# Optimization experiments

Hardware: AMD Instinct MI355X
Metric: run time of the kernel (lower is better)

Reference implementation:

```python
import jax, jax.numpy as jnp
import numpy as np

N_LOCAL = 16                      # top-k cone hits per (anchor, query)
COS_TH = float(np.cos(np.pi / 12))  # cone half-angle threshold: th = pi / cone_angle_th, cone_angle_th=12


def setup_inputs() -> dict:
    key = jax.random.key(0)
    k1, k2, k3 = jax.random.split(key, 3)
    pcd = jax.random.normal(k1, (2, 2048, 3), dtype=jnp.float32)  # point cloud
    qry = jax.random.normal(k2, (2, 512, 3), dtype=jnp.float32)   # query points
    anc = jax.random.normal(k3, (2, 48, 3), dtype=jnp.float32)    # anchors
    return {"pcd": pcd, "qry": qry, "anc": anc}


def reference(pcd, qry, anc):
    """Cone-cast top-k neighbor search + relative-feature computation of ARONetModel
    (cast_cone + cal_relatives with norm_coord=False), fully vectorized over anchors.

    Returns a single packed array [b, n_qry, n_anc, 1 + n_local, 4]:
      slot 0 along axis 3 is feat_anc2qry, slots 1..k are feat_qry2hit.
    """
    # ---- cast_cone (vectorized over the anchor loop of the original) ----
    # anchor->point distances/directions do NOT depend on the query, so compute once.
    vec_ap = pcd[:, None, :, :] - anc[:, :, None, :]            # [b,a,p,3]
    dist_ap = jnp.linalg.norm(vec_ap, axis=-1)                  # [b,a,p]
    dir_ap = vec_ap / dist_ap[..., None]                        # [b,a,p,3]

    vec_aq = qry[:, None, :, :] - anc[:, :, None, :]            # [b,a,q,3]
    dir_aq = vec_aq / jnp.linalg.norm(vec_aq, axis=-1, keepdims=True)

    # cosine between anchor->query ray and anchor->point directions
    cos = jnp.einsum('baqd,bapd->baqp', dir_aq, dir_ap)         # [b,a,q,p]
    # points outside the cone get distance +inf (torch: mod[flt_angle] = inf)
    masked = jnp.where(cos <= COS_TH, jnp.inf, dist_ap[:, :, None, :])  # [b,a,q,p]

    neg_vals, idx = jax.lax.top_k(-masked, N_LOCAL)             # smallest-k distances
    vals = -neg_vals                                            # [b,a,q,k]

    # gather the hit point coordinates
    hit_raw = jnp.take_along_axis(pcd[:, None, None, :, :], idx[..., None], axis=3)  # [b,a,q,k,3]
    # padded (no valid point in cone) -> replace with the query point itself
    pad = jnp.isinf(vals)[..., None]                            # [b,a,q,k,1]
    hit = jnp.where(pad, qry[:, None, :, None, :], hit_raw)     # [b,a,q,k,3]
    hit = jnp.transpose(hit, (0, 2, 1, 3, 4))                   # [b,q,a,k,3]

    # ---- cal_relatives (norm_coord = False) ----
    vec_qa = qry[:, :, None, :] - anc[:, None, :, :]            # [b,q,a,3]
    mod_qa = jnp.linalg.norm(vec_qa, axis=-1, keepdims=True)    # [b,q,a,1]
    feat_anc2qry = jnp.concatenate([vec_qa, mod_qa], axis=-1)   # [b,q,a,4]

    vec_qh = hit - qry[:, :, None, None, :]                     # [b,q,a,k,3]
    sq = jnp.sum(vec_qh * vec_qh, axis=-1, keepdims=True)       # [b,q,a,k,1]
    zero = sq == 0.0                                            # padded hits -> exact zero
    mod_qh = jnp.where(zero, 0.0, jnp.sqrt(jnp.where(zero, 1.0, sq)))
    feat_qry2hit = jnp.concatenate([vec_qh, mod_qh], axis=-1)   # [b,q,a,k,4]

    # pack both outputs into one array: [b,q,a,1+k,4]
    return jnp.concatenate([feat_anc2qry[:, :, :, None, :], feat_qry2hit], axis=3)
```

## Files before the change

kernel.cpp:

```cpp
#include <hip/hip_runtime.h>

#define P_N 2048
#define Q_N 512
#define A_N 48
#define WPTS 512
#define CHUNK 256
#define CAP 24
#define LSTR 25

__device__ __forceinline__ float dot3_rn(float ax, float ay, float az,
                                         float bx, float by, float bz) {
    return __fadd_rn(__fadd_rn(__fmul_rn(ax, bx), __fmul_rn(ay, by)),
                     __fmul_rn(az, bz));
}

__device__ __forceinline__ float dot3_fma(float ax, float ay, float az,
                                          float bx, float by, float bz) {
    return __fmaf_rn(az, bz, __fmaf_rn(ay, by, __fmul_rn(ax, bx)));
}

__device__ __forceinline__ void insert16(float d, int idx, float (&td)[16], int (&ti)[16]) {
    if (d >= td[15]) return;
    #pragma unroll
    for (int j = 15; j >= 1; --j) {
        float oldd = td[j]; int oldi = ti[j];
        bool up   = (d < td[j - 1]);
        bool here = (d < oldd);
        td[j] = up ? td[j - 1] : (here ? d : oldd);
        ti[j] = up ? ti[j - 1] : (here ? idx : oldi);
    }
    if (d < td[0]) { ti[0] = idx; td[0] = d; }
}

__global__ __launch_bounds__(256, 4) void aronet_kernel(
        const float* __restrict__ pcd, const float* __restrict__ qry,
        const float* __restrict__ anc, float* __restrict__ out) {
    __shared__ float4 spt[P_N];
    __shared__ unsigned char cand[256 * LSTR];

    uint2* mbuf = (uint2*)spt;

    const int tid  = threadIdx.x;
    const int lane = tid & 63;
    const int w    = tid >> 6;

    const int bid = blockIdx.x;
    const int qc  = bid & 7;
    const int ba  = bid >> 3;
    const int a   = ba % A_N;
    const int b   = ba / A_N;

    const float ax = anc[(b * A_N + a) * 3 + 0];
    const float ay = anc[(b * A_N + a) * 3 + 1];
    const float az = anc[(b * A_N + a) * 3 + 2];

    const float* pbase = pcd + (size_t)b * P_N * 3;
    const int pq0 = w * WPTS;
    for (int i = lane; i < WPTS; i += 64) {
        const int p = pq0 + i;
        float vx = __fsub_rn(pbase[p * 3 + 0], ax);
        float vy = __fsub_rn(pbase[p * 3 + 1], ay);
        float vz = __fsub_rn(pbase[p * 3 + 2], az);
        float d2 = dot3_rn(vx, vy, vz, vx, vy, vz);
        float dist = __fsqrt_rn(d2);
        float r = __fdiv_rn(1.0f, dist);
        spt[p] = make_float4(dist, __fmul_rn(vx, r), __fmul_rn(vy, r), __fmul_rn(vz, r));
    }

    const int q = (qc << 6) + lane;
    const float qx = qry[((size_t)b * Q_N + q) * 3 + 0];
    const float qy = qry[((size_t)b * Q_N + q) * 3 + 1];
    const float qz = qry[((size_t)b * Q_N + q) * 3 + 2];
    const float vqx = __fsub_rn(qx, ax);
    const float vqy = __fsub_rn(qy, ay);
    const float vqz = __fsub_rn(qz, az);
    const float qd2 = dot3_rn(vqx, vqy, vqz, vqx, vqy, vqz);
    const float qdist = __fsqrt_rn(qd2);
    const float qr = __fdiv_rn(1.0f, qdist);
    const float dqx = __fmul_rn(vqx, qr);
    const float dqy = __fmul_rn(vqy, qr);
    const float dqz = __fmul_rn(vqz, qr);

    const float COS_TH = 0.9659258262890683f;

    float td[16]; int ti[16];
    #pragma unroll
    for (int j = 0; j < 16; ++j) { td[j] = __builtin_inff(); ti[j] = 0; }

    const int lbase = tid * LSTR;
    int cnt = 0;
    for (int c0 = pq0; c0 < pq0 + WPTS; c0 += CHUNK) {
        #pragma unroll 8
        for (int p = c0; p < c0 + CHUNK; ++p) {
            float4 pt = spt[p];
            float cosv = dot3_fma(dqx, dqy, dqz, pt.y, pt.z, pt.w);
            if (!(cosv <= COS_TH)) {
                if (cnt < CAP) { cand[lbase + cnt] = (unsigned char)(p - c0); cnt++; }
                else insert16(pt.x, p, td, ti);
            }
        }
        for (int k = 0; k < cnt; ++k) {
            int i = c0 + cand[lbase + k];
            insert16(spt[i].x, i, td, ti);
        }
        cnt = 0;
    }

    __syncthreads();
    if (w > 0) {
        uint2* mb = mbuf + (w - 1) * 1024;
        #pragma unroll
        for (int k = 0; k < 16; ++k)
            mb[k * 64 + lane] = make_uint2(__float_as_uint(td[k]), (unsigned)ti[k]);
    }
    __syncthreads();

    if (w == 0) {
        for (int w2 = 0; w2 < 3; ++w2) {
            const uint2* mb = mbuf + w2 * 1024;
            #pragma unroll
            for (int k = 0; k < 16; ++k) {
                uint2 e = mb[k * 64 + lane];
                float d = __uint_as_float(e.x);
                if (d < __builtin_inff()) insert16(d, (int)e.y, td, ti);
            }
        }

        float4* o = (float4*)(out + (((size_t)(b * Q_N + q) * A_N + a) * 17) * 4);
        o[0] = make_float4(vqx, vqy, vqz, qdist);

        #pragma unroll
        for (int j = 0; j < 16; ++j) {
            float4 wv;
            if (td[j] == __builtin_inff()) {
                wv = make_float4(0.0f, 0.0f, 0.0f, 0.0f);
            } else {
                const float* hp = pbase + (size_t)ti[j] * 3;
                float hx = __fsub_rn(hp[0], qx);
                float hy = __fsub_rn(hp[1], qy);
                float hz = __fsub_rn(hp[2], qz);
                float sq = dot3_rn(hx, hy, hz, hx, hy, hz);
                float md = (sq == 0.0f) ? 0.0f : __fsqrt_rn(sq);
                wv = make_float4(hx, hy, hz, md);
            }
            o[1 + j] = wv;
        }
    }
}

extern "C" void kernel_launch(void* const* d_in, const int* in_sizes, int n_in,
                              void* d_out, int out_size, void* d_ws, size_t ws_size,
                              hipStream_t stream) {
    const float* pcd = (const float*)d_in[0];
    const float* qry = (const float*)d_in[1];
    const float* anc = (const float*)d_in[2];
    float* out = (float*)d_out;

    dim3 grid(2 * A_N * 8);
    dim3 block(256);
    hipLaunchKernelGGL(aronet_kernel, grid, block, 0, stream, pcd, qry, anc, out);
}
```

Before: 206.1 us.

## Broadcast precomputed point directions via readlane instead of LDS table

Each lane now precomputes 8 anchor-relative point directions in registers, and the cone test loop broadcasts them to all lanes with readlane rather than reading a float4 table from shared memory. The candidate buffer now stores (distance, index) pairs with a smaller capacity, so the flush step no longer re-reads the point table. This is meant to remove LDS read traffic and shrink shared memory use, which could allow more resident blocks. In exchange it adds scalar readlane instructions and register pressure, and a small candidate capacity means more direct insertions when the buffer overflows.

```diff
diff --git a/kernel.cpp b/kernel.cpp
--- a/kernel.cpp
+++ b/kernel.cpp
@@ -4,9 +4,8 @@
 #define Q_N 512
 #define A_N 48
 #define WPTS 512
-#define CHUNK 256
-#define CAP 24
-#define LSTR 25
+#define PPL 8
+#define CAP 13
 
 __device__ __forceinline__ float dot3_rn(float ax, float ay, float az,
                                          float bx, float by, float bz) {
@@ -32,13 +31,15 @@
     if (d < td[0]) { ti[0] = idx; td[0] = d; }
 }
 
+__device__ __forceinline__ float bcast(float v, int l) {
+    return __uint_as_float(__builtin_amdgcn_readlane(__float_as_uint(v), l));
+}
+
 __global__ __launch_bounds__(256, 4) void aronet_kernel(
         const float* __restrict__ pcd, const float* __restrict__ qry,
         const float* __restrict__ anc, float* __restrict__ out) {
-    __shared__ float4 spt[P_N];
-    __shared__ unsigned char cand[256 * LSTR];
-
-    uint2* mbuf = (uint2*)spt;
+    __shared__ uint2 cand[256 * CAP];
+    uint2* mbuf = cand;
 
     const int tid  = threadIdx.x;
     const int lane = tid & 63;
@@ -55,16 +56,22 @@
     const float az = anc[(b * A_N + a) * 3 + 2];
 
     const float* pbase = pcd + (size_t)b * P_N * 3;
-    const int pq0 = w * WPTS;
-    for (int i = lane; i < WPTS; i += 64) {
-        const int p = pq0 + i;
-        float vx = __fsub_rn(pbase[p * 3 + 0], ax);
-        float vy = __fsub_rn(pbase[p * 3 + 1], ay);
-        float vz = __fsub_rn(pbase[p * 3 + 2], az);
+    const int pq0  = w * WPTS;
+    const int myp0 = pq0 + lane * PPL;
+    float pd[PPL], pxv[PPL], pyv[PPL], pzv[PPL];
+    #pragma unroll
+    for (int s = 0; s < PPL; ++s) {
+        const float* pp = pbase + (size_t)(myp0 + s) * 3;
+        float vx = __fsub_rn(pp[0], ax);
+        float vy = __fsub_rn(pp[1], ay);
+        float vz = __fsub_rn(pp[2], az);
         float d2 = dot3_rn(vx, vy, vz, vx, vy, vz);
         float dist = __fsqrt_rn(d2);
         float r = __fdiv_rn(1.0f, dist);
-        spt[p] = make_float4(dist, __fmul_rn(vx, r), __fmul_rn(vy, r), __fmul_rn(vz, r));
+        pd[s]  = dist;
+        pxv[s] = __fmul_rn(vx, r);
+        pyv[s] = __fmul_rn(vy, r);
+        pzv[s] = __fmul_rn(vz, r);
     }
 
     const int q = (qc << 6) + lane;
@@ -87,21 +94,31 @@
     #pragma unroll
     for (int j = 0; j < 16; ++j) { td[j] = __builtin_inff(); ti[j] = 0; }
 
-    const int lbase = tid * LSTR;
+    const int lbase = tid * CAP;
     int cnt = 0;
-    for (int c0 = pq0; c0 < pq0 + WPTS; c0 += CHUNK) {
-        #pragma unroll 8
-        for (int p = c0; p < c0 + CHUNK; ++p) {
-            float4 pt = spt[p];
-            float cosv = dot3_fma(dqx, dqy, dqz, pt.y, pt.z, pt.w);
-            if (!(cosv <= COS_TH)) {
-                if (cnt < CAP) { cand[lbase + cnt] = (unsigned char)(p - c0); cnt++; }
-                else insert16(pt.x, p, td, ti);
+    for (int half = 0; half < 2; ++half) {
+        for (int L = half * 32; L < half * 32 + 32; ++L) {
+            #pragma unroll
+            for (int s = 0; s < PPL; ++s) {
+                float sd = bcast(pd[s],  L);
+                float sx = bcast(pxv[s], L);
+                float sy = bcast(pyv[s], L);
+                float sz = bcast(pzv[s], L);
+                float cosv = dot3_fma(dqx, dqy, dqz, sx, sy, sz);
+                if (!(cosv <= COS_TH)) {
+                    const int p = pq0 + L * PPL + s;
+                    if (cnt < CAP) {
+                        cand[lbase + cnt] = make_uint2(__float_as_uint(sd), (unsigned)p);
+                        ++cnt;
+                    } else {
+                        insert16(sd, p, td, ti);
+                    }
+                }
             }
         }
         for (int k = 0; k < cnt; ++k) {
-            int i = c0 + cand[lbase + k];
-            insert16(spt[i].x, i, td, ti);
+            uint2 e = cand[lbase + k];
+            insert16(__uint_as_float(e.x), (int)e.y, td, ti);
         }
         cnt = 0;
     }
```

After: 242.6 us. 1.18x slower.
